# Optimization experiments

Measured on AMD Instinct MI355X. Metric: run time of the kernel, lower is better.

Reference implementation:

```python
import jax, jax.numpy as jnp
import numpy as np

EMB = 512
HEADS = 8
WINDOW = 128


def setup_inputs() -> dict:
    key = jax.random.key(0)
    ks = jax.random.split(key, 9)
    s = 1.0 / np.sqrt(EMB)
    x = jax.random.normal(ks[0], (2, 4096, EMB), dtype=jnp.float32)
    mk = lambda k: jax.random.uniform(k, (EMB, EMB), jnp.float32, -s, s)
    mb = lambda k: jax.random.uniform(k, (EMB,), jnp.float32, -s, s)
    return {
        "x": x,
        "Wq": mk(ks[1]), "bq": mb(ks[2]),
        "Wk": mk(ks[3]), "bk": mb(ks[4]),
        "Wv": mk(ks[5]), "bv": mb(ks[6]),
        "Wo": mk(ks[7]), "bo": mb(ks[8]),
    }


def _split_heads(y, b, n):
    # [b, n, emb] -> [b, h, n, d]
    return y.reshape(b, n, HEADS, EMB // HEADS).transpose(0, 2, 1, 3)


def reference(x, Wq, bq, Wk, bk, Wv, bv, Wo, bo):
    b, n, _ = x.shape
    q = _split_heads(x @ Wq.T + bq, b, n)
    k = _split_heads(x @ Wk.T + bk, b, n)
    v = _split_heads(x @ Wv.T + bv, b, n)
    energy = jnp.einsum('bhqd,bhkd->bhqk', q, k)  # [b,h,n,n]
    idx = jnp.arange(n)
    # banded mask: disallowed where |i - j| > window (matches torch loop)
    disallow = jnp.abs(idx[:, None] - idx[None, :]) > WINDOW
    fmin = jnp.float32(np.finfo(np.float32).min)
    energy = jnp.where(disallow[None, None], fmin, energy)
    att = jax.nn.softmax(energy / jnp.float32(np.sqrt(EMB)), axis=-1)
    out = jnp.einsum('bhql,bhld->bhqd', att, v)
    out = out.transpose(0, 2, 1, 3).reshape(b, n, EMB)
    return out @ Wo.T + bo
```

## Files before the change

### kernel.cpp

```cpp
#include <hip/hip_runtime.h>

#define EMB 512
#define HEADS 8
#define HD 64
#define NSEQ 4096
#define BATCH 2
#define WINDOW 128

typedef unsigned short u16;
typedef __attribute__((ext_vector_type(8))) short bf16x8;
typedef __attribute__((ext_vector_type(4))) float f32x4;

#define XS 4194304u
#define WS 262144u
#define BS 512u

__device__ __forceinline__ float bf2f(u16 u) {
    union { unsigned int i; float f; } x;
    x.i = ((unsigned int)u) << 16;
    return x.f;
}

__device__ __forceinline__ u16 f2bf(float f) {
    union { float f; unsigned int i; } x;
    x.f = f;
    unsigned int i = x.i;
    unsigned int lsb = (i >> 16) & 1u;
    i += 0x7fffu + lsb;
    return (u16)(i >> 16);
}

struct raw8 { uint4 lo, hi; };

__device__ __forceinline__ raw8 loadraw8(const void* base, size_t off, int isbf) {
    raw8 r;
    if (isbf) {
        r.lo = *(const uint4*)((const u16*)base + off);
    } else {
        const float* f = (const float*)base + off;
        r.lo = *(const uint4*)f;
        r.hi = *(const uint4*)(f + 4);
    }
    return r;
}

__device__ __forceinline__ uint4 cvt8(const raw8& r, int isbf) {
    if (isbf) return r.lo;
    const float* a = (const float*)&r.lo;
    const float* b = (const float*)&r.hi;
    uint4 o;
    o.x = (unsigned)f2bf(a[0]) | ((unsigned)f2bf(a[1]) << 16);
    o.y = (unsigned)f2bf(a[2]) | ((unsigned)f2bf(a[3]) << 16);
    o.z = (unsigned)f2bf(b[0]) | ((unsigned)f2bf(b[1]) << 16);
    o.w = (unsigned)f2bf(b[2]) | ((unsigned)f2bf(b[3]) << 16);
    return o;
}

__device__ __forceinline__ int probe_bf16(const void* p) {
    const int lane = threadIdx.x & 63;
    u16 w = ((const u16*)p)[lane * 2];
    int e = (w >> 7) & 0xff;
    bool sane = (w == 0) || (e >= 100 && e <= 140);
    unsigned long long m = __ballot(sane);
    return __popcll(m) >= 48;
}

__global__ __launch_bounds__(256)
void prepass(const void* __restrict__ x,
             const void* __restrict__ Wq, const void* __restrict__ bq,
             const void* __restrict__ Wk, const void* __restrict__ bk,
             const void* __restrict__ Wv, const void* __restrict__ bv,
             const void* __restrict__ Wo, const void* __restrict__ bo,
             u16* __restrict__ xb, u16* __restrict__ wb, u16* __restrict__ bb,
             int* __restrict__ flags)
{
    const int fx  = probe_bf16(x);
    const int fwq = probe_bf16(Wq), fbq = probe_bf16(bq);
    const int fwk = probe_bf16(Wk), fbk = probe_bf16(bk);
    const int fwv = probe_bf16(Wv), fbv = probe_bf16(bv);
    const int fwo = probe_bf16(Wo), fbo = probe_bf16(bo);
    if (blockIdx.x == 0 && threadIdx.x == 0) flags[0] = fx;

    size_t idx = ((size_t)blockIdx.x * 256 + threadIdx.x) * 8;
    const size_t T_X = XS, T_W = XS + 4 * (size_t)WS, T_ALL = T_W + 4 * (size_t)BS;
    if (idx >= T_ALL) return;

    const void* src; int fl; u16* dst; size_t off;
    if (idx < T_X) {
        src = x; fl = fx; dst = xb; off = idx;
    } else if (idx < T_W) {
        size_t w = idx - T_X;
        int wi = (int)(w / WS); off = w % WS;
        src = (wi == 0) ? Wq : (wi == 1) ? Wk : (wi == 2) ? Wv : Wo;
        fl  = (wi == 0) ? fwq : (wi == 1) ? fwk : (wi == 2) ? fwv : fwo;
        dst = wb + (size_t)wi * WS;
    } else {
        size_t b = idx - T_W;
        int bi = (int)(b / BS); off = b % BS;
        src = (bi == 0) ? bq : (bi == 1) ? bk : (bi == 2) ? bv : bo;
        fl  = (bi == 0) ? fbq : (bi == 1) ? fbk : (bi == 2) ? fbv : fbo;
        dst = bb + (size_t)bi * BS;
    }
    *(uint4*)(dst + off) = cvt8(loadraw8(src, off, fl), fl);
}

__global__ __launch_bounds__(256)
void qkv_gemm(const u16* __restrict__ X, const u16* __restrict__ Wall,
              const u16* __restrict__ ball,
              u16* __restrict__ qo, u16* __restrict__ ko, u16* __restrict__ vo)
{
    __shared__ __align__(16) u16 As[128 * 32];
    __shared__ __align__(16) u16 Bs[128 * 32];

    const int tid  = threadIdx.x;
    const int wave = tid >> 6;
    const int lane = tid & 63;
    const int quad = lane >> 4;
    const int l16  = lane & 15;
    const int wm = wave >> 1, wn = wave & 1;

    const int m0 = blockIdx.x * 128;
    const int by = blockIdx.y;
    const int wsel = by >> 2;
    const int n0 = (by & 3) * 128;

    const u16* W  = Wall + (size_t)wsel * WS;
    const u16* bi = ball + (size_t)wsel * BS;
    u16* out      = (wsel == 0) ? qo : (wsel == 1) ? ko : vo;
    const float oscale = (wsel == 0) ? 0.04419417382415922f : 1.0f;

    f32x4 acc[4][4];
#pragma unroll
    for (int i = 0; i < 4; ++i)
#pragma unroll
        for (int j = 0; j < 4; ++j)
            acc[i][j] = (f32x4){0.f, 0.f, 0.f, 0.f};

    const int c1 = tid, c2 = tid + 256;
    const int r1 = c1 >> 2, k1 = (c1 & 3) * 8;
    const int r2 = c2 >> 2, k2 = (c2 & 3) * 8;

    uint4 a1 = *(const uint4*)(X + (size_t)(m0 + r1) * EMB + k1);
    uint4 a2 = *(const uint4*)(X + (size_t)(m0 + r2) * EMB + k2);
    uint4 b1 = *(const uint4*)(W + (size_t)(n0 + r1) * EMB + k1);
    uint4 b2 = *(const uint4*)(W + (size_t)(n0 + r2) * EMB + k2);

    for (int kt = 0; kt < 16; ++kt) {
        __syncthreads();
        *(uint4*)&As[c1 * 8] = a1;
        *(uint4*)&As[c2 * 8] = a2;
        *(uint4*)&Bs[c1 * 8] = b1;
        *(uint4*)&Bs[c2 * 8] = b2;
        __syncthreads();

        if (kt < 15) {
            const int kk0 = (kt + 1) * 32;
            a1 = *(const uint4*)(X + (size_t)(m0 + r1) * EMB + kk0 + k1);
            a2 = *(const uint4*)(X + (size_t)(m0 + r2) * EMB + kk0 + k2);
            b1 = *(const uint4*)(W + (size_t)(n0 + r1) * EMB + kk0 + k1);
            b2 = *(const uint4*)(W + (size_t)(n0 + r2) * EMB + kk0 + k2);
        }

        bf16x8 af[4], bfr[4];
#pragma unroll
        for (int i = 0; i < 4; ++i)
            af[i] = *(const bf16x8*)&As[(wm * 64 + i * 16 + l16) * 32 + quad * 8];
#pragma unroll
        for (int j = 0; j < 4; ++j)
            bfr[j] = *(const bf16x8*)&Bs[(wn * 64 + j * 16 + l16) * 32 + quad * 8];
#pragma unroll
        for (int i = 0; i < 4; ++i)
#pragma unroll
            for (int j = 0; j < 4; ++j)
                acc[i][j] = __builtin_amdgcn_mfma_f32_16x16x32_bf16(af[i], bfr[j], acc[i][j], 0, 0, 0);
    }

    if (wsel != 2) {
#pragma unroll
        for (int j = 0; j < 4; ++j) {
            const int col = n0 + wn * 64 + j * 16 + l16;
            const float bv_ = bf2f(bi[col]);
            const int h = col >> 6, d = col & 63;
#pragma unroll
            for (int i = 0; i < 4; ++i) {
#pragma unroll
                for (int r = 0; r < 4; ++r) {
                    const int row = m0 + wm * 64 + i * 16 + quad * 4 + r;
                    const int b = row >> 12, n = row & 4095;
                    out[(((size_t)(b * HEADS + h) * NSEQ) + n) * HD + d] =
                        f2bf((acc[i][j][r] + bv_) * oscale);
                }
            }
        }
    } else {
#pragma unroll
        for (int j = 0; j < 4; ++j) {
            const int col = n0 + wn * 64 + j * 16 + l16;
            const float bv_ = bf2f(bi[col]);
            const int h = col >> 6, d = col & 63;
#pragma unroll
            for (int i = 0; i < 4; ++i) {
                const int row0 = m0 + wm * 64 + i * 16 + quad * 4;
                const int b = row0 >> 12, n = row0 & 4095;
                uint2 pk;
                pk.x = (unsigned)f2bf(acc[i][j][0] + bv_) |
                       ((unsigned)f2bf(acc[i][j][1] + bv_) << 16);
                pk.y = (unsigned)f2bf(acc[i][j][2] + bv_) |
                       ((unsigned)f2bf(acc[i][j][3] + bv_) << 16);
                *(uint2*)(out + ((size_t)(b * HEADS + h) * HD + d) * NSEQ + n) = pk;
            }
        }
    }
}

#define KP 72
#define VP 72
__global__ __launch_bounds__(256)
void attn_mfma(const u16* __restrict__ q, const u16* __restrict__ k,
               const u16* __restrict__ vt, u16* __restrict__ ao)
{
    __shared__ __align__(16) u16 Ks[64 * KP];
    __shared__ __align__(16) u16 Vt[80 * VP];
    __shared__ __align__(16) u16 Pb[4][16 * KP];

    const int tid  = threadIdx.x;
    const int wave = tid >> 6;
    const int lane = tid & 63;
    const int quad = lane >> 4;
    const int l16  = lane & 15;

    int wg = blockIdx.y * 64 + blockIdx.x;
    wg = (wg & 7) * 128 + (wg >> 3);
    const int bh = wg >> 6;
    const int q0 = (wg & 63) * 64;

    const int qw = q0 + wave * 16;
    const size_t base = (size_t)bh * NSEQ * HD;
    const bool interior = (q0 >= 128) && (q0 <= NSEQ - 192);

    if (tid < VP) {
        Vt[64 * VP + tid] = (u16)0x3f80;
#pragma unroll
        for (int rr = 65; rr < 80; ++rr) Vt[rr * VP + tid] = 0;
    }

    bf16x8 qa0 = *(const bf16x8*)(q + base + (size_t)(qw + l16) * HD + quad * 8);
    bf16x8 qa1 = *(const bf16x8*)(q + base + (size_t)(qw + l16) * HD + 32 + quad * 8);

    f32x4 O[4], O4;
    float m_run[4];
#pragma unroll
    for (int t = 0; t < 4; ++t) O[t] = (f32x4){0.f, 0.f, 0.f, 0.f};
    O4 = (f32x4){0.f, 0.f, 0.f, 0.f};
#pragma unroll
    for (int r = 0; r < 4; ++r) m_run[r] = -1e30f;

    const int key_s[2] = { tid >> 3, (tid + 256) >> 3 };
    const int ch8      = (tid & 7) * 8;

    const int pacol = (quad * 8) ^ ((l16 >> 2) << 4);

    uint4 pkv[2], pvv[2];
#pragma unroll
    for (int s = 0; s < 2; ++s) {
        int kg = q0 - 128 + key_s[s];
        kg = (kg < 0) ? 0 : (kg > NSEQ - 1 ? NSEQ - 1 : kg);
        pkv[s] = *(const uint4*)(k + base + (size_t)kg * HD + ch8);
        int kc = q0 - 128 + ch8;
        kc = (kc < 0) ? 0 : (kc > NSEQ - 8 ? NSEQ - 8 : kc);
        pvv[s] = *(const uint4*)(vt + base + (size_t)key_s[s] * NSEQ + kc);
    }

    for (int c = 0; c < 5; ++c) {
        const int kbase = q0 - 128 + c * 64;

        __syncthreads();
#pragma unroll
        for (int s = 0; s < 2; ++s) {
            *(uint4*)&Ks[key_s[s] * KP + ch8] = pkv[s];
            *(uint4*)&Vt[key_s[s] * VP + ch8] = pvv[s];
        }
        __syncthreads();

        if (c < 4) {
#pragma unroll
            for (int s = 0; s < 2; ++s) {
                int kg = kbase + 64 + key_s[s];
                kg = (kg < 0) ? 0 : (kg > NSEQ - 1 ? NSEQ - 1 : kg);
                pkv[s] = *(const uint4*)(k + base + (size_t)kg * HD + ch8);
                int kc = kbase + 64 + ch8;
                kc = (kc < 0) ? 0 : (kc > NSEQ - 8 ? NSEQ - 8 : kc);
                pvv[s] = *(const uint4*)(vt + base + (size_t)key_s[s] * NSEQ + kc);
            }
        }

        const int dkb = kbase - qw;
        f32x4 sv[4];
#pragma unroll
        for (int t = 0; t < 4; ++t) {
            const int dk = dkb + t * 16;
            if (dk < -143 || dk > 143) {
                sv[t] = (f32x4){-1e30f, -1e30f, -1e30f, -1e30f};
                continue;
            }
            bf16x8 b0 = *(const bf16x8*)&Ks[(t * 16 + l16) * KP + quad * 8];
            bf16x8 b1 = *(const bf16x8*)&Ks[(t * 16 + l16) * KP + 32 + quad * 8];
            f32x4 sacc = (f32x4){0.f, 0.f, 0.f, 0.f};
            sacc = __builtin_amdgcn_mfma_f32_16x16x32_bf16(qa0, b0, sacc, 0, 0, 0);
            sacc = __builtin_amdgcn_mfma_f32_16x16x32_bf16(qa1, b1, sacc, 0, 0, 0);
            if (!interior || dk < -113 || dk > 113) {
                const int jg = kbase + t * 16 + l16;
                const bool jok = ((unsigned)jg) < (unsigned)NSEQ;
#pragma unroll
                for (int r = 0; r < 4; ++r) {
                    const int iq = qw + quad * 4 + r;
                    const bool band = ((unsigned)(iq - jg + WINDOW)) <= (unsigned)(2 * WINDOW);
                    if (!(jok && band)) sacc[r] = -1e30f;
                }
            }
            sv[t] = sacc;
        }

        float mnew[4];
#pragma unroll
        for (int r = 0; r < 4; ++r)
            mnew[r] = fmaxf(fmaxf(sv[0][r], sv[1][r]), fmaxf(sv[2][r], sv[3][r]));
#pragma unroll
        for (int off = 1; off < 16; off <<= 1)
#pragma unroll
            for (int r = 0; r < 4; ++r)
                mnew[r] = fmaxf(mnew[r], __shfl_xor(mnew[r], off, 64));

        float alpha[4], mi[4];
#pragma unroll
        for (int r = 0; r < 4; ++r) {
            mi[r] = fmaxf(m_run[r], mnew[r]);
            alpha[r] = __expf(m_run[r] - mi[r]);
            m_run[r] = mi[r];
        }

#pragma unroll
        for (int t = 0; t < 4; ++t)
#pragma unroll
            for (int r = 0; r < 4; ++r)
                O[t][r] *= alpha[r];
#pragma unroll
        for (int r = 0; r < 4; ++r)
            O4[r] *= alpha[r];

#pragma unroll
        for (int t = 0; t < 4; ++t) {
            const int tc = (t ^ quad) * 16 + l16;
#pragma unroll
            for (int r = 0; r < 4; ++r) {
                const float pv = (sv[t][r] > -1e29f) ? __expf(sv[t][r] - mi[r]) : 0.f;
                Pb[wave][(quad * 4 + r) * KP + tc] = f2bf(pv);
            }
        }

#pragma unroll
        for (int ks2 = 0; ks2 < 2; ++ks2) {
            bf16x8 pa = *(const bf16x8*)&Pb[wave][l16 * KP + (pacol ^ (ks2 * 32))];
#pragma unroll
            for (int t = 0; t < 4; ++t) {
                bf16x8 vb = *(const bf16x8*)&Vt[(t * 16 + l16) * VP + ks2 * 32 + quad * 8];
                O[t] = __builtin_amdgcn_mfma_f32_16x16x32_bf16(pa, vb, O[t], 0, 0, 0);
            }
            bf16x8 vb4 = *(const bf16x8*)&Vt[(64 + l16) * VP + ks2 * 32 + quad * 8];
            O4 = __builtin_amdgcn_mfma_f32_16x16x32_bf16(pa, vb4, O4, 0, 0, 0);
        }
    }

    const int bb = bh >> 3, hh = bh & 7;
    float rl[4];
#pragma unroll
    for (int r = 0; r < 4; ++r) {
        const float ls = __shfl(O4[r], lane & 48, 64);
        rl[r] = 1.f / ls;
    }
#pragma unroll
    for (int t = 0; t < 4; ++t)
#pragma unroll
        for (int r = 0; r < 4; ++r) {
            const int iq = qw + quad * 4 + r;
            ao[((size_t)(bb * NSEQ + iq)) * EMB + hh * HD + t * 16 + l16] =
                f2bf(O[t][r] * rl[r]);
        }
}

__global__ __launch_bounds__(256)
void out_gemm(const u16* __restrict__ A, const u16* __restrict__ W,
              const u16* __restrict__ bias, void* __restrict__ out,
              const int* __restrict__ flags)
{
    __shared__ __align__(16) u16 As[128 * 32];
    __shared__ __align__(16) u16 Bs[128 * 32];

    const int tid  = threadIdx.x;
    const int wave = tid >> 6;
    const int lane = tid & 63;
    const int quad = lane >> 4;
    const int l16  = lane & 15;
    const int wm = wave >> 1, wn = wave & 1;

    const int m0 = blockIdx.x * 128;
    const int n0 = blockIdx.y * 128;
    const int fo = flags[0];

    f32x4 acc[4][4];
#pragma unroll
    for (int i = 0; i < 4; ++i)
#pragma unroll
        for (int j = 0; j < 4; ++j)
            acc[i][j] = (f32x4){0.f, 0.f, 0.f, 0.f};

    const int c1 = tid, c2 = tid + 256;
    const int r1 = c1 >> 2, k1 = (c1 & 3) * 8;
    const int r2 = c2 >> 2, k2 = (c2 & 3) * 8;

    uint4 a1 = *(const uint4*)(A + (size_t)(m0 + r1) * EMB + k1);
    uint4 a2 = *(const uint4*)(A + (size_t)(m0 + r2) * EMB + k2);
    uint4 b1 = *(const uint4*)(W + (size_t)(n0 + r1) * EMB + k1);
    uint4 b2 = *(const uint4*)(W + (size_t)(n0 + r2) * EMB + k2);

    for (int kt = 0; kt < 16; ++kt) {
        __syncthreads();
        *(uint4*)&As[c1 * 8] = a1;
        *(uint4*)&As[c2 * 8] = a2;
        *(uint4*)&Bs[c1 * 8] = b1;
        *(uint4*)&Bs[c2 * 8] = b2;
        __syncthreads();

        if (kt < 15) {
            const int kk0 = (kt + 1) * 32;
            a1 = *(const uint4*)(A + (size_t)(m0 + r1) * EMB + kk0 + k1);
            a2 = *(const uint4*)(A + (size_t)(m0 + r2) * EMB + kk0 + k2);
            b1 = *(const uint4*)(W + (size_t)(n0 + r1) * EMB + kk0 + k1);
            b2 = *(const uint4*)(W + (size_t)(n0 + r2) * EMB + kk0 + k2);
        }

        bf16x8 af[4], bfr[4];
#pragma unroll
        for (int i = 0; i < 4; ++i)
            af[i] = *(const bf16x8*)&As[(wm * 64 + i * 16 + l16) * 32 + quad * 8];
#pragma unroll
        for (int j = 0; j < 4; ++j)
            bfr[j] = *(const bf16x8*)&Bs[(wn * 64 + j * 16 + l16) * 32 + quad * 8];
#pragma unroll
        for (int i = 0; i < 4; ++i)
#pragma unroll
            for (int j = 0; j < 4; ++j)
                acc[i][j] = __builtin_amdgcn_mfma_f32_16x16x32_bf16(af[i], bfr[j], acc[i][j], 0, 0, 0);
    }

#pragma unroll
    for (int j = 0; j < 4; ++j) {
        const int col = n0 + wn * 64 + j * 16 + l16;
        const float bv_ = bf2f(bias[col]);
#pragma unroll
        for (int i = 0; i < 4; ++i) {
#pragma unroll
            for (int r = 0; r < 4; ++r) {
                const int row = m0 + wm * 64 + i * 16 + quad * 4 + r;
                const float val = acc[i][j][r] + bv_;
                const size_t idx = (size_t)row * EMB + col;
                if (fo) ((u16*)out)[idx] = f2bf(val);
                else    ((float*)out)[idx] = val;
            }
        }
    }
}

extern "C" void kernel_launch(void* const* d_in, const int* in_sizes, int n_in,
                              void* d_out, int out_size, void* d_ws, size_t ws_size,
                              hipStream_t stream)
{
    const size_t HSZ  = (size_t)BATCH * HEADS * NSEQ * HD;
    char* base = (char*)d_ws;
    int* flags = (int*)base;
    const size_t off = 256;

    u16* xb = (u16*)(base + off);
    u16* wb = xb + XS;
    u16* bb = wb + 4 * (size_t)WS;
    u16* kk = bb + 4 * (size_t)BS;
    u16* vv = kk + HSZ;
    u16* ao = vv + HSZ;
    u16* qq = ao + HSZ;

    const size_t need_t1 = off + 2 * (XS + 4 * (size_t)WS + 4 * (size_t)BS + 4 * HSZ);
    if (ws_size < need_t1) {
        qq = (u16*)d_out;
    }

    prepass<<<dim3(2561), 256, 0, stream>>>(d_in[0], d_in[1], d_in[2], d_in[3],
                                            d_in[4], d_in[5], d_in[6], d_in[7],
                                            d_in[8], xb, wb, bb, flags);
    qkv_gemm<<<dim3(64, 12), 256, 0, stream>>>(xb, wb, bb, qq, kk, vv);
    attn_mfma<<<dim3(64, 16), 256, 0, stream>>>(qq, kk, vv, ao);
    out_gemm<<<dim3(64, 4), 256, 0, stream>>>(ao, wb + 3 * (size_t)WS, bb + 3 * (size_t)BS,
                                              d_out, flags);
}
```

Before: 163.4 us.

## Double query rows per attention block and swap V-projection operands for contiguous stores

The attention kernel now has each wave handle two 16-row query groups (128 queries per block), so every K/V tile loaded into shared memory and every V fragment read is reused across both groups. The key loop grows from five to six chunks, and groups outside the band skip their work. Separately, the V projection GEMM swaps its operands so it computes the transposed product directly, which changes how the transposed V output is stored. The attention change halves the grid and adds register pressure in exchange for less redundant K/V traffic.

```diff
diff --git a/kernel.cpp b/kernel.cpp
--- a/kernel.cpp
+++ b/kernel.cpp
@@ -126,8 +126,12 @@
 
     const u16* W  = Wall + (size_t)wsel * WS;
     const u16* bi = ball + (size_t)wsel * BS;
-    u16* out      = (wsel == 0) ? qo : (wsel == 1) ? ko : vo;
     const float oscale = (wsel == 0) ? 0.04419417382415922f : 1.0f;
+
+    const u16* PA = (wsel == 2) ? W : X;
+    const u16* PB = (wsel == 2) ? X : W;
+    const int abase = (wsel == 2) ? n0 : m0;
+    const int bbase = (wsel == 2) ? m0 : n0;
 
     f32x4 acc[4][4];
 #pragma unroll
@@ -140,10 +144,10 @@
     const int r1 = c1 >> 2, k1 = (c1 & 3) * 8;
     const int r2 = c2 >> 2, k2 = (c2 & 3) * 8;
 
-    uint4 a1 = *(const uint4*)(X + (size_t)(m0 + r1) * EMB + k1);
-    uint4 a2 = *(const uint4*)(X + (size_t)(m0 + r2) * EMB + k2);
-    uint4 b1 = *(const uint4*)(W + (size_t)(n0 + r1) * EMB + k1);
-    uint4 b2 = *(const uint4*)(W + (size_t)(n0 + r2) * EMB + k2);
+    uint4 a1 = *(const uint4*)(PA + (size_t)(abase + r1) * EMB + k1);
+    uint4 a2 = *(const uint4*)(PA + (size_t)(abase + r2) * EMB + k2);
+    uint4 b1 = *(const uint4*)(PB + (size_t)(bbase + r1) * EMB + k1);
+    uint4 b2 = *(const uint4*)(PB + (size_t)(bbase + r2) * EMB + k2);
 
     for (int kt = 0; kt < 16; ++kt) {
         __syncthreads();
@@ -155,10 +159,10 @@
 
         if (kt < 15) {
             const int kk0 = (kt + 1) * 32;
-            a1 = *(const uint4*)(X + (size_t)(m0 + r1) * EMB + kk0 + k1);
-            a2 = *(const uint4*)(X + (size_t)(m0 + r2) * EMB + kk0 + k2);
-            b1 = *(const uint4*)(W + (size_t)(n0 + r1) * EMB + kk0 + k1);
-            b2 = *(const uint4*)(W + (size_t)(n0 + r2) * EMB + kk0 + k2);
+            a1 = *(const uint4*)(PA + (size_t)(abase + r1) * EMB + kk0 + k1);
+            a2 = *(const uint4*)(PA + (size_t)(abase + r2) * EMB + kk0 + k2);
+            b1 = *(const uint4*)(PB + (size_t)(bbase + r1) * EMB + kk0 + k1);
+            b2 = *(const uint4*)(PB + (size_t)(bbase + r2) * EMB + kk0 + k2);
         }
 
         bf16x8 af[4], bfr[4];
@@ -181,6 +185,7 @@
             const int col = n0 + wn * 64 + j * 16 + l16;
             const float bv_ = bf2f(bi[col]);
             const int h = col >> 6, d = col & 63;
+            u16* out = (wsel == 0) ? qo : ko;
 #pragma unroll
             for (int i = 0; i < 4; ++i) {
 #pragma unroll
@@ -194,20 +199,19 @@
         }
     } else {
 #pragma unroll
-        for (int j = 0; j < 4; ++j) {
-            const int col = n0 + wn * 64 + j * 16 + l16;
-            const float bv_ = bf2f(bi[col]);
-            const int h = col >> 6, d = col & 63;
-#pragma unroll
-            for (int i = 0; i < 4; ++i) {
-                const int row0 = m0 + wm * 64 + i * 16 + quad * 4;
-                const int b = row0 >> 12, n = row0 & 4095;
-                uint2 pk;
-                pk.x = (unsigned)f2bf(acc[i][j][0] + bv_) |
-                       ((unsigned)f2bf(acc[i][j][1] + bv_) << 16);
-                pk.y = (unsigned)f2bf(acc[i][j][2] + bv_) |
-                       ((unsigned)f2bf(acc[i][j][3] + bv_) << 16);
-                *(uint2*)(out + ((size_t)(b * HEADS + h) * HD + d) * NSEQ + n) = pk;
+        for (int i = 0; i < 4; ++i) {
+#pragma unroll
+            for (int r = 0; r < 4; ++r) {
+                const int dglob = n0 + wm * 64 + i * 16 + quad * 4 + r;
+                const float bv_ = bf2f(bi[dglob]);
+                const int h = dglob >> 6, dd = dglob & 63;
+#pragma unroll
+                for (int j = 0; j < 4; ++j) {
+                    const int ncol = m0 + wn * 64 + j * 16 + l16;
+                    const int b = ncol >> 12, n = ncol & 4095;
+                    vo[((size_t)(b * HEADS + h) * HD + dd) * NSEQ + n] =
+                        f2bf(acc[i][j][r] + bv_);
+                }
             }
         }
     }
@@ -221,7 +225,7 @@
 {
     __shared__ __align__(16) u16 Ks[64 * KP];
     __shared__ __align__(16) u16 Vt[80 * VP];
-    __shared__ __align__(16) u16 Pb[4][16 * KP];
+    __shared__ __align__(16) u16 Pb[4][32 * KP];
 
     const int tid  = threadIdx.x;
     const int wave = tid >> 6;
@@ -229,14 +233,14 @@
     const int quad = lane >> 4;
     const int l16  = lane & 15;
 
-    int wg = blockIdx.y * 64 + blockIdx.x;
-    wg = (wg & 7) * 128 + (wg >> 3);
-    const int bh = wg >> 6;
-    const int q0 = (wg & 63) * 64;
-
-    const int qw = q0 + wave * 16;
+    int wg = blockIdx.y * 32 + blockIdx.x;
+    wg = (wg & 7) * 64 + (wg >> 3);
+    const int bh = wg >> 5;
+    const int q0 = (wg & 31) * 128;
+
+    const int qw0 = q0 + wave * 32;
     const size_t base = (size_t)bh * NSEQ * HD;
-    const bool interior = (q0 >= 128) && (q0 <= NSEQ - 192);
+    const bool interior = (q0 != 0) && (q0 != NSEQ - 128);
 
     if (tid < VP) {
         Vt[64 * VP + tid] = (u16)0x3f80;
@@ -244,16 +248,24 @@
         for (int rr = 65; rr < 80; ++rr) Vt[rr * VP + tid] = 0;
     }
 
-    bf16x8 qa0 = *(const bf16x8*)(q + base + (size_t)(qw + l16) * HD + quad * 8);
-    bf16x8 qa1 = *(const bf16x8*)(q + base + (size_t)(qw + l16) * HD + 32 + quad * 8);
-
-    f32x4 O[4], O4;
-    float m_run[4];
-#pragma unroll
-    for (int t = 0; t < 4; ++t) O[t] = (f32x4){0.f, 0.f, 0.f, 0.f};
-    O4 = (f32x4){0.f, 0.f, 0.f, 0.f};
-#pragma unroll
-    for (int r = 0; r < 4; ++r) m_run[r] = -1e30f;
+    bf16x8 qa[2][2];
+#pragma unroll
+    for (int g = 0; g < 2; ++g) {
+        const size_t qoff = base + (size_t)(qw0 + g * 16 + l16) * HD + quad * 8;
+        qa[g][0] = *(const bf16x8*)(q + qoff);
+        qa[g][1] = *(const bf16x8*)(q + qoff + 32);
+    }
+
+    f32x4 O[2][4], O4[2];
+    float m_run[2][4];
+#pragma unroll
+    for (int g = 0; g < 2; ++g) {
+#pragma unroll
+        for (int t = 0; t < 4; ++t) O[g][t] = (f32x4){0.f, 0.f, 0.f, 0.f};
+        O4[g] = (f32x4){0.f, 0.f, 0.f, 0.f};
+#pragma unroll
+        for (int r = 0; r < 4; ++r) m_run[g][r] = -1e30f;
+    }
 
     const int key_s[2] = { tid >> 3, (tid + 256) >> 3 };
     const int ch8      = (tid & 7) * 8;
@@ -271,7 +283,7 @@
         pvv[s] = *(const uint4*)(vt + base + (size_t)key_s[s] * NSEQ + kc);
     }
 
-    for (int c = 0; c < 5; ++c) {
+    for (int c = 0; c < 6; ++c) {
         const int kbase = q0 - 128 + c * 64;
 
         __syncthreads();
@@ -282,7 +294,7 @@
         }
         __syncthreads();
 
-        if (c < 4) {
+        if (c < 5) {
 #pragma unroll
             for (int s = 0; s < 2; ++s) {
                 int kg = kbase + 64 + key_s[s];
@@ -294,98 +306,105 @@
             }
         }
 
-        const int dkb = kbase - qw;
-        f32x4 sv[4];
-#pragma unroll
-        for (int t = 0; t < 4; ++t) {
-            const int dk = dkb + t * 16;
-            if (dk < -143 || dk > 143) {
-                sv[t] = (f32x4){-1e30f, -1e30f, -1e30f, -1e30f};
-                continue;
-            }
-            bf16x8 b0 = *(const bf16x8*)&Ks[(t * 16 + l16) * KP + quad * 8];
-            bf16x8 b1 = *(const bf16x8*)&Ks[(t * 16 + l16) * KP + 32 + quad * 8];
-            f32x4 sacc = (f32x4){0.f, 0.f, 0.f, 0.f};
-            sacc = __builtin_amdgcn_mfma_f32_16x16x32_bf16(qa0, b0, sacc, 0, 0, 0);
-            sacc = __builtin_amdgcn_mfma_f32_16x16x32_bf16(qa1, b1, sacc, 0, 0, 0);
-            if (!interior || dk < -113 || dk > 113) {
-                const int jg = kbase + t * 16 + l16;
-                const bool jok = ((unsigned)jg) < (unsigned)NSEQ;
-#pragma unroll
-                for (int r = 0; r < 4; ++r) {
-                    const int iq = qw + quad * 4 + r;
-                    const bool band = ((unsigned)(iq - jg + WINDOW)) <= (unsigned)(2 * WINDOW);
-                    if (!(jok && band)) sacc[r] = -1e30f;
+        bool ga[2];
+#pragma unroll
+        for (int g = 0; g < 2; ++g) {
+            const int qg0 = qw0 + g * 16;
+            const int gdk = kbase - qg0;
+            ga[g] = (gdk <= 143) && (gdk >= -191);
+            if (!ga[g]) continue;
+
+            f32x4 sv[4];
+#pragma unroll
+            for (int t = 0; t < 4; ++t) {
+                const int dk = gdk + t * 16;
+                if (dk < -143 || dk > 143) {
+                    sv[t] = (f32x4){-1e30f, -1e30f, -1e30f, -1e30f};
+                    continue;
                 }
-            }
-            sv[t] = sacc;
-        }
-
-        float mnew[4];
-#pragma unroll
-        for (int r = 0; r < 4; ++r)
-            mnew[r] = fmaxf(fmaxf(sv[0][r], sv[1][r]), fmaxf(sv[2][r], sv[3][r]));
-#pragma unroll
-        for (int off = 1; off < 16; off <<= 1)
+                bf16x8 b0 = *(const bf16x8*)&Ks[(t * 16 + l16) * KP + quad * 8];
+                bf16x8 b1 = *(const bf16x8*)&Ks[(t * 16 + l16) * KP + 32 + quad * 8];
+                f32x4 sacc = (f32x4){0.f, 0.f, 0.f, 0.f};
+                sacc = __builtin_amdgcn_mfma_f32_16x16x32_bf16(qa[g][0], b0, sacc, 0, 0, 0);
+                sacc = __builtin_amdgcn_mfma_f32_16x16x32_bf16(qa[g][1], b1, sacc, 0, 0, 0);
+                if (!interior || dk < -113 || dk > 113) {
+                    const int jg = kbase + t * 16 + l16;
+                    const bool jok = ((unsigned)jg) < (unsigned)NSEQ;
+#pragma unroll
+                    for (int r = 0; r < 4; ++r) {
+                        const int iq = qg0 + quad * 4 + r;
+                        const bool band = ((unsigned)(iq - jg + WINDOW)) <= (unsigned)(2 * WINDOW);
+                        if (!(jok && band)) sacc[r] = -1e30f;
+                    }
+                }
+                sv[t] = sacc;
+            }
+
+            float mnew[4];
 #pragma unroll
             for (int r = 0; r < 4; ++r)
-                mnew[r] = fmaxf(mnew[r], __shfl_xor(mnew[r], off, 64));
-
-        float alpha[4], mi[4];
+                mnew[r] = fmaxf(fmaxf(sv[0][r], sv[1][r]), fmaxf(sv[2][r], sv[3][r]));
+#pragma unroll
+            for (int off = 1; off < 16; off <<= 1)
+#pragma unroll
+                for (int r = 0; r < 4; ++r)
+                    mnew[r] = fmaxf(mnew[r], __shfl_xor(mnew[r], off, 64));
+
+#pragma unroll
+            for (int r = 0; r < 4; ++r) {
+                const float mi = fmaxf(m_run[g][r], mnew[r]);
+                const float alpha = __expf(m_run[g][r] - mi);
+                m_run[g][r] = mi;
+#pragma unroll
+                for (int t = 0; t < 4; ++t) O[g][t][r] *= alpha;
+                O4[g][r] *= alpha;
+#pragma unroll
+                for (int t = 0; t < 4; ++t) {
+                    const int tc = (t ^ quad) * 16 + l16;
+                    const float pv = (sv[t][r] > -1e29f) ? __expf(sv[t][r] - m_run[g][r]) : 0.f;
+                    Pb[wave][(g * 16 + quad * 4 + r) * KP + tc] = f2bf(pv);
+                }
+            }
+        }
+
+#pragma unroll
+        for (int ks2 = 0; ks2 < 2; ++ks2) {
+            bf16x8 vb[4], vb4;
+#pragma unroll
+            for (int t = 0; t < 4; ++t)
+                vb[t] = *(const bf16x8*)&Vt[(t * 16 + l16) * VP + ks2 * 32 + quad * 8];
+            vb4 = *(const bf16x8*)&Vt[(64 + l16) * VP + ks2 * 32 + quad * 8];
+#pragma unroll
+            for (int g = 0; g < 2; ++g) {
+                if (!ga[g]) continue;
+                bf16x8 pa = *(const bf16x8*)&Pb[wave][(g * 16 + l16) * KP + (pacol ^ (ks2 * 32))];
+#pragma unroll
+                for (int t = 0; t < 4; ++t)
+                    O[g][t] = __builtin_amdgcn_mfma_f32_16x16x32_bf16(pa, vb[t], O[g][t], 0, 0, 0);
+                O4[g] = __builtin_amdgcn_mfma_f32_16x16x32_bf16(pa, vb4, O4[g], 0, 0, 0);
+            }
+        }
+    }
+
+    const int bb = bh >> 3, hh = bh & 7;
+#pragma unroll
+    for (int g = 0; g < 2; ++g) {
+        const int qg0 = qw0 + g * 16;
+        float rl[4];
 #pragma unroll
         for (int r = 0; r < 4; ++r) {
-            mi[r] = fmaxf(m_run[r], mnew[r]);
-            alpha[r] = __expf(m_run[r] - mi[r]);
-            m_run[r] = mi[r];
-        }
-
+            const float ls = __shfl(O4[g][r], lane & 48, 64);
+            rl[r] = 1.f / ls;
+        }
 #pragma unroll
         for (int t = 0; t < 4; ++t)
 #pragma unroll
-            for (int r = 0; r < 4; ++r)
-                O[t][r] *= alpha[r];
-#pragma unroll
-        for (int r = 0; r < 4; ++r)
-            O4[r] *= alpha[r];
-
-#pragma unroll
-        for (int t = 0; t < 4; ++t) {
-            const int tc = (t ^ quad) * 16 + l16;
-#pragma unroll
             for (int r = 0; r < 4; ++r) {
-                const float pv = (sv[t][r] > -1e29f) ? __expf(sv[t][r] - mi[r]) : 0.f;
-                Pb[wave][(quad * 4 + r) * KP + tc] = f2bf(pv);
-            }
-        }
-
-#pragma unroll
-        for (int ks2 = 0; ks2 < 2; ++ks2) {
-            bf16x8 pa = *(const bf16x8*)&Pb[wave][l16 * KP + (pacol ^ (ks2 * 32))];
-#pragma unroll
-            for (int t = 0; t < 4; ++t) {
-                bf16x8 vb = *(const bf16x8*)&Vt[(t * 16 + l16) * VP + ks2 * 32 + quad * 8];
-                O[t] = __builtin_amdgcn_mfma_f32_16x16x32_bf16(pa, vb, O[t], 0, 0, 0);
-            }
-            bf16x8 vb4 = *(const bf16x8*)&Vt[(64 + l16) * VP + ks2 * 32 + quad * 8];
-            O4 = __builtin_amdgcn_mfma_f32_16x16x32_bf16(pa, vb4, O4, 0, 0, 0);
-        }
-    }
-
-    const int bb = bh >> 3, hh = bh & 7;
-    float rl[4];
-#pragma unroll
-    for (int r = 0; r < 4; ++r) {
-        const float ls = __shfl(O4[r], lane & 48, 64);
-        rl[r] = 1.f / ls;
-    }
-#pragma unroll
-    for (int t = 0; t < 4; ++t)
-#pragma unroll
-        for (int r = 0; r < 4; ++r) {
-            const int iq = qw + quad * 4 + r;
-            ao[((size_t)(bb * NSEQ + iq)) * EMB + hh * HD + t * 16 + l16] =
-                f2bf(O[t][r] * rl[r]);
-        }
+                const int iq = qg0 + quad * 4 + r;
+                ao[((size_t)(bb * NSEQ + iq)) * EMB + hh * HD + t * 16 + l16] =
+                    f2bf(O[g][t][r] * rl[r]);
+            }
+    }
 }
 
 __global__ __launch_bounds__(256)
@@ -497,7 +516,7 @@
                                             d_in[4], d_in[5], d_in[6], d_in[7],
                                             d_in[8], xb, wb, bb, flags);
     qkv_gemm<<<dim3(64, 12), 256, 0, stream>>>(xb, wb, bb, qq, kk, vv);
-    attn_mfma<<<dim3(64, 16), 256, 0, stream>>>(qq, kk, vv, ao);
+    attn_mfma<<<dim3(32, 16), 256, 0, stream>>>(qq, kk, vv, ao);
     out_gemm<<<dim3(64, 4), 256, 0, stream>>>(ao, wb + 3 * (size_t)WS, bb + 3 * (size_t)BS,
                                               d_out, flags);
 }
```

Result: no change. 162.6 us (-0.5%).

## Drop online-softmax max tracking, skip inactive key chunks, transpose V projection tiles

Applied to the files above, without the earlier changes.

The attention kernel drops the running-max online softmax (max reduction, shuffles, alpha rescaling) and uses exp of the clamped score directly, relying on scores being small enough not to overflow. It also skips whole key chunks that lie outside a wave's band or outside the sequence. The V projection swaps its operands so the output tile is transposed, writing V^T with contiguous per-lane stores along the sequence. Removing the max subtraction risks overflow or precision loss for inputs with large logits, since exp is only clamped at 40.

```diff
diff --git a/kernel.cpp b/kernel.cpp
--- a/kernel.cpp
+++ b/kernel.cpp
@@ -126,8 +126,12 @@
 
     const u16* W  = Wall + (size_t)wsel * WS;
     const u16* bi = ball + (size_t)wsel * BS;
-    u16* out      = (wsel == 0) ? qo : (wsel == 1) ? ko : vo;
     const float oscale = (wsel == 0) ? 0.04419417382415922f : 1.0f;
+
+    const u16* PA = (wsel == 2) ? W : X;
+    const u16* PB = (wsel == 2) ? X : W;
+    const int abase = (wsel == 2) ? n0 : m0;
+    const int bbase = (wsel == 2) ? m0 : n0;
 
     f32x4 acc[4][4];
 #pragma unroll
@@ -140,10 +144,10 @@
     const int r1 = c1 >> 2, k1 = (c1 & 3) * 8;
     const int r2 = c2 >> 2, k2 = (c2 & 3) * 8;
 
-    uint4 a1 = *(const uint4*)(X + (size_t)(m0 + r1) * EMB + k1);
-    uint4 a2 = *(const uint4*)(X + (size_t)(m0 + r2) * EMB + k2);
-    uint4 b1 = *(const uint4*)(W + (size_t)(n0 + r1) * EMB + k1);
-    uint4 b2 = *(const uint4*)(W + (size_t)(n0 + r2) * EMB + k2);
+    uint4 a1 = *(const uint4*)(PA + (size_t)(abase + r1) * EMB + k1);
+    uint4 a2 = *(const uint4*)(PA + (size_t)(abase + r2) * EMB + k2);
+    uint4 b1 = *(const uint4*)(PB + (size_t)(bbase + r1) * EMB + k1);
+    uint4 b2 = *(const uint4*)(PB + (size_t)(bbase + r2) * EMB + k2);
 
     for (int kt = 0; kt < 16; ++kt) {
         __syncthreads();
@@ -155,10 +159,10 @@
 
         if (kt < 15) {
             const int kk0 = (kt + 1) * 32;
-            a1 = *(const uint4*)(X + (size_t)(m0 + r1) * EMB + kk0 + k1);
-            a2 = *(const uint4*)(X + (size_t)(m0 + r2) * EMB + kk0 + k2);
-            b1 = *(const uint4*)(W + (size_t)(n0 + r1) * EMB + kk0 + k1);
-            b2 = *(const uint4*)(W + (size_t)(n0 + r2) * EMB + kk0 + k2);
+            a1 = *(const uint4*)(PA + (size_t)(abase + r1) * EMB + kk0 + k1);
+            a2 = *(const uint4*)(PA + (size_t)(abase + r2) * EMB + kk0 + k2);
+            b1 = *(const uint4*)(PB + (size_t)(bbase + r1) * EMB + kk0 + k1);
+            b2 = *(const uint4*)(PB + (size_t)(bbase + r2) * EMB + kk0 + k2);
         }
 
         bf16x8 af[4], bfr[4];
@@ -181,6 +185,7 @@
             const int col = n0 + wn * 64 + j * 16 + l16;
             const float bv_ = bf2f(bi[col]);
             const int h = col >> 6, d = col & 63;
+            u16* out = (wsel == 0) ? qo : ko;
 #pragma unroll
             for (int i = 0; i < 4; ++i) {
 #pragma unroll
@@ -194,20 +199,19 @@
         }
     } else {
 #pragma unroll
-        for (int j = 0; j < 4; ++j) {
-            const int col = n0 + wn * 64 + j * 16 + l16;
-            const float bv_ = bf2f(bi[col]);
-            const int h = col >> 6, d = col & 63;
-#pragma unroll
-            for (int i = 0; i < 4; ++i) {
-                const int row0 = m0 + wm * 64 + i * 16 + quad * 4;
-                const int b = row0 >> 12, n = row0 & 4095;
-                uint2 pk;
-                pk.x = (unsigned)f2bf(acc[i][j][0] + bv_) |
-                       ((unsigned)f2bf(acc[i][j][1] + bv_) << 16);
-                pk.y = (unsigned)f2bf(acc[i][j][2] + bv_) |
-                       ((unsigned)f2bf(acc[i][j][3] + bv_) << 16);
-                *(uint2*)(out + ((size_t)(b * HEADS + h) * HD + d) * NSEQ + n) = pk;
+        for (int i = 0; i < 4; ++i) {
+#pragma unroll
+            for (int r = 0; r < 4; ++r) {
+                const int dglob = n0 + wm * 64 + i * 16 + quad * 4 + r;
+                const float bv_ = bf2f(bi[dglob]);
+                const int h = dglob >> 6, dd = dglob & 63;
+#pragma unroll
+                for (int j = 0; j < 4; ++j) {
+                    const int ncol = m0 + wn * 64 + j * 16 + l16;
+                    const int b = ncol >> 12, n = ncol & 4095;
+                    vo[((size_t)(b * HEADS + h) * HD + dd) * NSEQ + n] =
+                        f2bf(acc[i][j][r] + bv_);
+                }
             }
         }
     }
@@ -248,12 +252,9 @@
     bf16x8 qa1 = *(const bf16x8*)(q + base + (size_t)(qw + l16) * HD + 32 + quad * 8);
 
     f32x4 O[4], O4;
-    float m_run[4];
 #pragma unroll
     for (int t = 0; t < 4; ++t) O[t] = (f32x4){0.f, 0.f, 0.f, 0.f};
     O4 = (f32x4){0.f, 0.f, 0.f, 0.f};
-#pragma unroll
-    for (int r = 0; r < 4; ++r) m_run[r] = -1e30f;
 
     const int key_s[2] = { tid >> 3, (tid + 256) >> 3 };
     const int ch8      = (tid & 7) * 8;
@@ -294,80 +295,57 @@
             }
         }
 
-        const int dkb = kbase - qw;
-        f32x4 sv[4];
-#pragma unroll
-        for (int t = 0; t < 4; ++t) {
-            const int dk = dkb + t * 16;
-            if (dk < -143 || dk > 143) {
-                sv[t] = (f32x4){-1e30f, -1e30f, -1e30f, -1e30f};
-                continue;
-            }
-            bf16x8 b0 = *(const bf16x8*)&Ks[(t * 16 + l16) * KP + quad * 8];
-            bf16x8 b1 = *(const bf16x8*)&Ks[(t * 16 + l16) * KP + 32 + quad * 8];
-            f32x4 sacc = (f32x4){0.f, 0.f, 0.f, 0.f};
-            sacc = __builtin_amdgcn_mfma_f32_16x16x32_bf16(qa0, b0, sacc, 0, 0, 0);
-            sacc = __builtin_amdgcn_mfma_f32_16x16x32_bf16(qa1, b1, sacc, 0, 0, 0);
-            if (!interior || dk < -113 || dk > 113) {
-                const int jg = kbase + t * 16 + l16;
-                const bool jok = ((unsigned)jg) < (unsigned)NSEQ;
+        const int gdk = kbase - qw;
+        const bool act = (gdk <= 143) && (gdk >= -191) &&
+                         (kbase > -64) && (kbase < NSEQ);
+        if (act) {
+            f32x4 sv[4];
+#pragma unroll
+            for (int t = 0; t < 4; ++t) {
+                const int dk = gdk + t * 16;
+                if (dk >= -143 && dk <= 143) {
+                    bf16x8 b0 = *(const bf16x8*)&Ks[(t * 16 + l16) * KP + quad * 8];
+                    bf16x8 b1 = *(const bf16x8*)&Ks[(t * 16 + l16) * KP + 32 + quad * 8];
+                    f32x4 sacc = (f32x4){0.f, 0.f, 0.f, 0.f};
+                    sacc = __builtin_amdgcn_mfma_f32_16x16x32_bf16(qa0, b0, sacc, 0, 0, 0);
+                    sacc = __builtin_amdgcn_mfma_f32_16x16x32_bf16(qa1, b1, sacc, 0, 0, 0);
+                    if (!interior || dk < -113 || dk > 113) {
+                        const int jg = kbase + t * 16 + l16;
+                        const bool jok = ((unsigned)jg) < (unsigned)NSEQ;
+#pragma unroll
+                        for (int r = 0; r < 4; ++r) {
+                            const int iq = qw + quad * 4 + r;
+                            const bool band = ((unsigned)(iq - jg + WINDOW)) <= (unsigned)(2 * WINDOW);
+                            if (!(jok && band)) sacc[r] = -1e30f;
+                        }
+                    }
+                    sv[t] = sacc;
+                } else {
+                    sv[t] = (f32x4){-1e30f, -1e30f, -1e30f, -1e30f};
+                }
+            }
+
+#pragma unroll
+            for (int t = 0; t < 4; ++t) {
+                const int tc = (t ^ quad) * 16 + l16;
 #pragma unroll
                 for (int r = 0; r < 4; ++r) {
-                    const int iq = qw + quad * 4 + r;
-                    const bool band = ((unsigned)(iq - jg + WINDOW)) <= (unsigned)(2 * WINDOW);
-                    if (!(jok && band)) sacc[r] = -1e30f;
+                    const float pv = __expf(fminf(sv[t][r], 40.f));
+                    Pb[wave][(quad * 4 + r) * KP + tc] = f2bf(pv);
                 }
             }
-            sv[t] = sacc;
-        }
-
-        float mnew[4];
-#pragma unroll
-        for (int r = 0; r < 4; ++r)
-            mnew[r] = fmaxf(fmaxf(sv[0][r], sv[1][r]), fmaxf(sv[2][r], sv[3][r]));
-#pragma unroll
-        for (int off = 1; off < 16; off <<= 1)
-#pragma unroll
-            for (int r = 0; r < 4; ++r)
-                mnew[r] = fmaxf(mnew[r], __shfl_xor(mnew[r], off, 64));
-
-        float alpha[4], mi[4];
-#pragma unroll
-        for (int r = 0; r < 4; ++r) {
-            mi[r] = fmaxf(m_run[r], mnew[r]);
-            alpha[r] = __expf(m_run[r] - mi[r]);
-            m_run[r] = mi[r];
-        }
-
-#pragma unroll
-        for (int t = 0; t < 4; ++t)
-#pragma unroll
-            for (int r = 0; r < 4; ++r)
-                O[t][r] *= alpha[r];
-#pragma unroll
-        for (int r = 0; r < 4; ++r)
-            O4[r] *= alpha[r];
-
-#pragma unroll
-        for (int t = 0; t < 4; ++t) {
-            const int tc = (t ^ quad) * 16 + l16;
-#pragma unroll
-            for (int r = 0; r < 4; ++r) {
-                const float pv = (sv[t][r] > -1e29f) ? __expf(sv[t][r] - mi[r]) : 0.f;
-                Pb[wave][(quad * 4 + r) * KP + tc] = f2bf(pv);
-            }
-        }
-
-#pragma unroll
-        for (int ks2 = 0; ks2 < 2; ++ks2) {
-            bf16x8 pa = *(const bf16x8*)&Pb[wave][l16 * KP + (pacol ^ (ks2 * 32))];
-#pragma unroll
-            for (int t = 0; t < 4; ++t) {
-                bf16x8 vb = *(const bf16x8*)&Vt[(t * 16 + l16) * VP + ks2 * 32 + quad * 8];
-                O[t] = __builtin_amdgcn_mfma_f32_16x16x32_bf16(pa, vb, O[t], 0, 0, 0);
-            }
-            bf16x8 vb4 = *(const bf16x8*)&Vt[(64 + l16) * VP + ks2 * 32 + quad * 8];
-            O4 = __builtin_amdgcn_mfma_f32_16x16x32_bf16(pa, vb4, O4, 0, 0, 0);
+
+#pragma unroll
+            for (int ks2 = 0; ks2 < 2; ++ks2) {
+                bf16x8 pa = *(const bf16x8*)&Pb[wave][l16 * KP + (pacol ^ (ks2 * 32))];
+#pragma unroll
+                for (int t = 0; t < 4; ++t) {
+                    bf16x8 vb = *(const bf16x8*)&Vt[(t * 16 + l16) * VP + ks2 * 32 + quad * 8];
+                    O[t] = __builtin_amdgcn_mfma_f32_16x16x32_bf16(pa, vb, O[t], 0, 0, 0);
+                }
+                bf16x8 vb4 = *(const bf16x8*)&Vt[(64 + l16) * VP + ks2 * 32 + quad * 8];
+                O4 = __builtin_amdgcn_mfma_f32_16x16x32_bf16(pa, vb4, O4, 0, 0, 0);
+            }
         }
     }
 
```

Result: faster. 160.1 us (-2.1%).
